# Kernel optimization log

Hardware: AMD Instinct MI355X
Metric: run time of the kernel (lower is better)

The kernel has to match this reference:

```python
import jax, jax.numpy as jnp
import numpy as np

EMBED = 1024
HEADS = 16
HEAD_DIM = EMBED // HEADS


def setup_inputs() -> dict:
    key = jax.random.key(0)
    ks = jax.random.split(key, 8)
    N, S, E = 4, 2048, EMBED
    s = 1.0 / np.sqrt(E)
    return {
        "values": jax.random.normal(ks[0], (N, S, E), jnp.float32),
        "keys": jax.random.normal(ks[1], (N, S, E), jnp.float32),
        "queries": jax.random.normal(ks[2], (N, S, E), jnp.float32),
        # nn.Linear weights stored as (out_features, in_features)
        "Wv": jax.random.normal(ks[3], (E, E), jnp.float32) * s,
        "Wk": jax.random.normal(ks[4], (E, E), jnp.float32) * s,
        "Wq": jax.random.normal(ks[5], (E, E), jnp.float32) * s,
        "Wo": jax.random.normal(ks[6], (E, E), jnp.float32) * s,
        "bo": jax.random.normal(ks[7], (E,), jnp.float32) * s,
    }


def reference(values, keys, queries, Wv, Wk, Wq, Wo, bo):
    N = queries.shape[0]
    H, D, E = HEADS, HEAD_DIM, EMBED
    # projections (torch Linear: x @ W.T), reshape to [N, S, H, D]
    v = (values @ Wv.T).reshape(N, -1, H, D)
    k = (keys @ Wk.T).reshape(N, -1, H, D)
    q = (queries @ Wq.T).reshape(N, -1, H, D)
    energy = jnp.einsum("nqhd,nkhd->nhqk", q, k)
    # NOTE: original scales by sqrt(embed_size), not sqrt(head_dim)
    attn = jax.nn.softmax(energy / jnp.sqrt(jnp.float32(E)), axis=3)
    out = jnp.einsum("nhql,nlhd->nqhd", attn, v).reshape(N, -1, H * D)
    return out @ Wo.T + bo
```

## Files before the change

### kernel.cpp

```cpp
#include <hip/hip_runtime.h>

typedef __bf16  bf16x8 __attribute__((ext_vector_type(8)));
typedef float   f32x4  __attribute__((ext_vector_type(4)));
typedef unsigned short u16x8 __attribute__((ext_vector_type(8)));

__device__ __forceinline__ unsigned short f2bf(float f) {
    union { float f; unsigned int u; } v; v.f = f;
    unsigned int u = v.u;
    unsigned int r = (u + 0x7fffu + ((u >> 16) & 1u)) >> 16;
    return (unsigned short)r;
}

__device__ __forceinline__ unsigned int pkbf(float lo, float hi) {
    union { float f; unsigned int u; } a, b; a.f = lo; b.f = hi;
    return __builtin_amdgcn_perm(b.u + 0x8000u, a.u + 0x8000u, 0x07060302u);
}

__device__ __forceinline__ void gld_lds16(const unsigned short* g, unsigned short* l) {
    auto gp = (const __attribute__((address_space(1))) unsigned int*)(const void*)g;
    auto lp = (__attribute__((address_space(3))) unsigned int*)(unsigned int)(unsigned long long)(void*)l;
    __builtin_amdgcn_global_load_lds(gp, lp, 16, 0, 0);
}

__global__ void cast4_kernel(const float* __restrict__ a, const float* __restrict__ b,
                             const float* __restrict__ c, const float* __restrict__ d,
                             unsigned short* __restrict__ dst) {
    int sel = blockIdx.x >> 10;
    int off4 = (blockIdx.x & 1023) * 256 + threadIdx.x;
    const float* src = sel == 0 ? a : sel == 1 ? b : sel == 2 ? c : d;
    float4 f = ((const float4*)src)[off4];
    uint2 pk; pk.x = pkbf(f.x, f.y); pk.y = pkbf(f.z, f.w);
    ((uint2*)(dst + (size_t)sel * 1048576))[off4] = pk;
}

__global__ void cast_kernel(const float* __restrict__ src, unsigned short* __restrict__ dst, int n4) {
    int stride = gridDim.x * 256;
    for (int i = blockIdx.x * 256 + threadIdx.x; i < n4; i += stride) {
        float4 f = ((const float4*)src)[i];
        uint2 pk; pk.x = pkbf(f.x, f.y); pk.y = pkbf(f.z, f.w);
        ((uint2*)dst)[i] = pk;
    }
}

template <int MODE>
__global__ __launch_bounds__(256, 3)
void gemm_bt(const unsigned short* __restrict__ A, const unsigned short* __restrict__ Bt,
             void* __restrict__ dst, const float* __restrict__ bias, float a_scale)
{
    constexpr int K = 1024;
    __shared__ unsigned short As[2][4096];
    __shared__ unsigned short Bs[2][4096];

    const int t    = threadIdx.x;
    const int lane = t & 63;
    const int w    = t >> 6;
    const int q    = lane >> 4;
    const int ln   = lane & 15;
    const int wr   = w >> 1, wc = w & 1;
    const int m0   = blockIdx.x * 128;
    const int n0   = blockIdx.y * 128;
    const int srow = lane >> 2;
    const int scol = (lane & 3) * 8;

    f32x4 acc[4][4];
    const f32x4 zz = {0.f, 0.f, 0.f, 0.f};
#pragma unroll
    for (int i = 0; i < 4; ++i)
#pragma unroll
        for (int j = 0; j < 4; ++j) acc[i][j] = zz;

    auto stage = [&](int k0, int p) {
#pragma unroll
        for (int c = 0; c < 2; ++c) {
            int u = w * 2 + c;
            gld_lds16(A  + (size_t)(m0 + u * 16 + srow) * K + k0 + scol, &As[p][u * 512]);
            gld_lds16(Bt + (size_t)(n0 + u * 16 + srow) * K + k0 + scol, &Bs[p][u * 512]);
        }
    };

    stage(0, 0);
    for (int j = 0; j < 32; ++j) {
        __syncthreads();
        if (j < 31) stage((j + 1) * 32, (j + 1) & 1);
        const int p = j & 1;
        bf16x8 af[4], bfr[4];
#pragma unroll
        for (int i = 0; i < 4; ++i)
            af[i] = *(const bf16x8*)&As[p][(wr * 64 + i * 16 + ln) * 32 + q * 8];
#pragma unroll
        for (int jj = 0; jj < 4; ++jj)
            bfr[jj] = *(const bf16x8*)&Bs[p][(wc * 64 + jj * 16 + ln) * 32 + q * 8];
#pragma unroll
        for (int i = 0; i < 4; ++i)
#pragma unroll
            for (int jj = 0; jj < 4; ++jj)
                acc[i][jj] = __builtin_amdgcn_mfma_f32_16x16x32_bf16(af[i], bfr[jj], acc[i][jj], 0, 0, 0);
    }

#pragma unroll
    for (int i = 0; i < 4; ++i) {
#pragma unroll
        for (int j = 0; j < 4; ++j) {
            f32x4 c = acc[i][j];
            int mb = m0 + wr * 64 + i * 16 + q * 4;
            int nn = n0 + wc * 64 + j * 16 + ln;
            if constexpr (MODE == 1) {
                int b = mb >> 11, s = mb & 2047, h = nn >> 6, d = nn & 63;
                uint2 pk;
                pk.x = pkbf(c[0], c[1]);
                pk.y = pkbf(c[2], c[3]);
                size_t idx = (((size_t)(b * 16 + h) * 64) + d) * 2048 + s;
                *(uint2*)&((unsigned short*)dst)[idx] = pk;
            } else {
#pragma unroll
                for (int r = 0; r < 4; ++r) {
                    int m = mb + r;
                    float val = c[r] * a_scale;
                    if constexpr (MODE == 2) {
                        ((float*)dst)[(size_t)m * 1024 + nn] = val + bias[nn];
                    } else {
                        int b = m >> 11, s = m & 2047, h = nn >> 6, d = nn & 63;
                        size_t idx = (((size_t)(b * 16 + h) * 2048) + s) * 64 + d;
                        ((unsigned short*)dst)[idx] = f2bf(val);
                    }
                }
            }
        }
    }
}

__global__ __launch_bounds__(256, 3)
void attn_kernel(const unsigned short* __restrict__ Q, const unsigned short* __restrict__ Kg,
                 const unsigned short* __restrict__ Vt, unsigned short* __restrict__ Og)
{
    __shared__ unsigned short Ks[2][4096];
    __shared__ unsigned short Vs[2][4096];
    __shared__ unsigned short Ps[128 * 72];

    const int t    = threadIdx.x;
    const int lane = t & 63;
    const int w    = t >> 6;
    const int q    = lane >> 4;
    const int ln   = lane & 15;
    const int head = blockIdx.x;
    const int qt   = blockIdx.y;

    const unsigned short* Qh  = Q  + (size_t)head * 2048 * 64;
    const unsigned short* Kh  = Kg + (size_t)head * 2048 * 64;
    const unsigned short* Vth = Vt + (size_t)head * 64 * 2048;

    const int srow = lane >> 2;
    const int scol = (lane & 3) * 8;

    bf16x8 qf[2][2];
    const int rowb = qt * 128 + w * 32;
#pragma unroll
    for (int ti = 0; ti < 2; ++ti)
#pragma unroll
        for (int kc = 0; kc < 2; ++kc)
            qf[ti][kc] = *(const bf16x8*)&Qh[(size_t)(rowb + ti * 16 + ln) * 64 + kc * 32 + q * 8];

    const f32x4 zz = {0.f, 0.f, 0.f, 0.f};
    f32x4 oa[2][4];
#pragma unroll
    for (int ti = 0; ti < 2; ++ti)
#pragma unroll
        for (int dt = 0; dt < 4; ++dt) oa[ti][dt] = zz;
    float l_s[2] = {0.f, 0.f};

    auto stage = [&](int j, int p) {
#pragma unroll
        for (int c = 0; c < 2; ++c) {
            int u = w * 2 + c;
            int kc = u >> 2, rg = u & 3;
            gld_lds16(Kh + (size_t)(j * 64 + rg * 16 + srow) * 64 + kc * 32 + scol,
                      &Ks[p][kc * 2048 + rg * 512]);
            gld_lds16(Vth + (size_t)(rg * 16 + srow) * 2048 + j * 64 + kc * 32 + scol,
                      &Vs[p][kc * 2048 + rg * 512]);
        }
    };

    stage(0, 0);
    for (int j = 0; j < 32; ++j) {
        __syncthreads();
        if (j < 31) stage(j + 1, (j + 1) & 1);
        const int p = j & 1;

        f32x4 sa[4][2];
#pragma unroll
        for (int kt = 0; kt < 4; ++kt)
#pragma unroll
            for (int ti = 0; ti < 2; ++ti) sa[kt][ti] = zz;
#pragma unroll
        for (int kc = 0; kc < 2; ++kc) {
            bf16x8 ka[4];
#pragma unroll
            for (int kt = 0; kt < 4; ++kt)
                ka[kt] = *(const bf16x8*)&Ks[p][kc * 2048 + (kt * 16 + ln) * 32 + q * 8];
#pragma unroll
            for (int kt = 0; kt < 4; ++kt)
#pragma unroll
                for (int ti = 0; ti < 2; ++ti)
                    sa[kt][ti] = __builtin_amdgcn_mfma_f32_16x16x32_bf16(ka[kt], qf[ti][kc], sa[kt][ti], 0, 0, 0);
        }

#pragma unroll
        for (int ti = 0; ti < 2; ++ti) {
            float rs = 0.f;
            const int prow = w * 32 + ti * 16 + ln;
#pragma unroll
            for (int kt = 0; kt < 4; ++kt) {
                float p0 = exp2f(sa[kt][ti][0]);
                float p1 = exp2f(sa[kt][ti][1]);
                float p2 = exp2f(sa[kt][ti][2]);
                float p3 = exp2f(sa[kt][ti][3]);
                rs += (p0 + p1) + (p2 + p3);
                uint2 pk;
                pk.x = pkbf(p0, p1);
                pk.y = pkbf(p2, p3);
                *(uint2*)&Ps[prow * 72 + kt * 16 + q * 4] = pk;
            }
            rs += __shfl_xor(rs, 16);
            rs += __shfl_xor(rs, 32);
            l_s[ti] += rs;
        }

#pragma unroll
        for (int kc = 0; kc < 2; ++kc) {
            bf16x8 va[4], pb[2];
#pragma unroll
            for (int dt = 0; dt < 4; ++dt)
                va[dt] = *(const bf16x8*)&Vs[p][kc * 2048 + (dt * 16 + ln) * 32 + q * 8];
#pragma unroll
            for (int ti = 0; ti < 2; ++ti)
                pb[ti] = *(const bf16x8*)&Ps[(w * 32 + ti * 16 + ln) * 72 + kc * 32 + q * 8];
#pragma unroll
            for (int ti = 0; ti < 2; ++ti)
#pragma unroll
                for (int dt = 0; dt < 4; ++dt)
                    oa[ti][dt] = __builtin_amdgcn_mfma_f32_16x16x32_bf16(va[dt], pb[ti], oa[ti][dt], 0, 0, 0);
        }
    }

    const int n = head >> 4;
    const int hbase = (head & 15) * 64;
#pragma unroll
    for (int ti = 0; ti < 2; ++ti) {
        float inv = 1.f / l_s[ti];
        int sr = qt * 128 + w * 32 + ti * 16 + ln;
        size_t base = ((size_t)n * 2048 + sr) * 1024 + hbase;
#pragma unroll
        for (int dt = 0; dt < 4; ++dt) {
            uint2 pk;
            pk.x = pkbf(oa[ti][dt][0] * inv, oa[ti][dt][1] * inv);
            pk.y = pkbf(oa[ti][dt][2] * inv, oa[ti][dt][3] * inv);
            *(uint2*)&Og[base + dt * 16 + q * 4] = pk;
        }
    }
}

extern "C" void kernel_launch(void* const* d_in, const int* in_sizes, int n_in,
                              void* d_out, int out_size, void* d_ws, size_t ws_size,
                              hipStream_t stream)
{
    (void)in_sizes; (void)n_in; (void)out_size; (void)ws_size;
    const float* values  = (const float*)d_in[0];
    const float* keys    = (const float*)d_in[1];
    const float* queries = (const float*)d_in[2];
    const float* Wv = (const float*)d_in[3];
    const float* Wk = (const float*)d_in[4];
    const float* Wq = (const float*)d_in[5];
    const float* Wo = (const float*)d_in[6];
    const float* bo = (const float*)d_in[7];
    float* out = (float*)d_out;

    unsigned short* ws   = (unsigned short*)d_ws;
    unsigned short* Wv_b = ws;
    unsigned short* Wk_b = ws + 1048576;
    unsigned short* Wq_b = ws + 2097152;
    unsigned short* Wo_b = ws + 3145728;
    unsigned short* Act  = ws + 4194304;
    unsigned short* Ob   = Act;
    unsigned short* Qb   = ws + 12582912;
    unsigned short* Kb   = Qb + 8388608;
    unsigned short* Vtb  = Kb + 8388608;

    cast4_kernel<<<4096, 256, 0, stream>>>(Wv, Wk, Wq, Wo, ws);

    dim3 g(64, 8), b(256);
    const float qscale = 1.4426950408889634f / 32.f;

    cast_kernel<<<4096, 256, 0, stream>>>(values, Act, 2097152);
    gemm_bt<1><<<g, b, 0, stream>>>(Act, Wv_b, Vtb, nullptr, 1.f);
    cast_kernel<<<4096, 256, 0, stream>>>(keys, Act, 2097152);
    gemm_bt<0><<<g, b, 0, stream>>>(Act, Wk_b, Kb, nullptr, 1.f);
    cast_kernel<<<4096, 256, 0, stream>>>(queries, Act, 2097152);
    gemm_bt<0><<<g, b, 0, stream>>>(Act, Wq_b, Qb, nullptr, qscale);

    attn_kernel<<<dim3(64, 16), b, 0, stream>>>(Qb, Kb, Vtb, Ob);
    gemm_bt<2><<<g, b, 0, stream>>>(Ob, Wo_b, out, bo, 1.f);
}
```

Before: 370.2 us.

## Keep softmax probabilities in registers and swizzle K/V shared-memory layout

Removes the Ps shared-memory staging buffer by feeding exp'd scores straight from the QK MFMA accumulators into 16x16x16 bf16 MFMAs for the PV product. It also XOR-swizzles the K/V tiles in LDS to avoid bank conflicts and raises the occupancy hint from 3 to 5 blocks per CU. This cuts LDS traffic and a write/read round trip per tile. The trade is twice as many smaller-K MFMA instructions for PV, plus round-to-nearest conversion via convertvector.

```diff
diff --git a/kernel.cpp b/kernel.cpp
--- a/kernel.cpp
+++ b/kernel.cpp
@@ -1,6 +1,8 @@
 #include <hip/hip_runtime.h>
 
 typedef __bf16  bf16x8 __attribute__((ext_vector_type(8)));
+typedef __bf16  bf16x4 __attribute__((ext_vector_type(4)));
+typedef short   s16x4  __attribute__((ext_vector_type(4)));
 typedef float   f32x4  __attribute__((ext_vector_type(4)));
 typedef unsigned short u16x8 __attribute__((ext_vector_type(8)));
 
@@ -20,6 +22,18 @@
     auto gp = (const __attribute__((address_space(1))) unsigned int*)(const void*)g;
     auto lp = (__attribute__((address_space(3))) unsigned int*)(unsigned int)(unsigned long long)(void*)l;
     __builtin_amdgcn_global_load_lds(gp, lp, 16, 0, 0);
+}
+
+__device__ __forceinline__ f32x4 mfma16(bf16x4 a, bf16x4 b, f32x4 c) {
+#if __has_builtin(__builtin_amdgcn_mfma_f32_16x16x16_bf16)
+    return __builtin_amdgcn_mfma_f32_16x16x16_bf16(a, b, c, 0, 0, 0);
+#elif __has_builtin(__builtin_amdgcn_mfma_f32_16x16x16bf16_1k)
+    union U { bf16x4 h; s16x4 s; } ua, ub; ua.h = a; ub.h = b;
+    return __builtin_amdgcn_mfma_f32_16x16x16bf16_1k(ua.s, ub.s, c, 0, 0, 0);
+#else
+    asm("v_mfma_f32_16x16x16_bf16 %0, %1, %2, %0" : "+v"(c) : "v"(a), "v"(b));
+    return c;
+#endif
 }
 
 __global__ void cast4_kernel(const float* __restrict__ a, const float* __restrict__ b,
@@ -129,19 +143,19 @@
     }
 }
 
-__global__ __launch_bounds__(256, 3)
+__global__ __launch_bounds__(256, 5)
 void attn_kernel(const unsigned short* __restrict__ Q, const unsigned short* __restrict__ Kg,
                  const unsigned short* __restrict__ Vt, unsigned short* __restrict__ Og)
 {
-    __shared__ unsigned short Ks[2][4096];
-    __shared__ unsigned short Vs[2][4096];
-    __shared__ unsigned short Ps[128 * 72];
+    __shared__ __align__(16) unsigned short Ks[2][4096];
+    __shared__ __align__(16) unsigned short Vs[2][4096];
 
     const int t    = threadIdx.x;
     const int lane = t & 63;
     const int w    = t >> 6;
     const int q    = lane >> 4;
     const int ln   = lane & 15;
+    const int xs   = (ln >> 1) & 3;
     const int head = blockIdx.x;
     const int qt   = blockIdx.y;
 
@@ -150,7 +164,7 @@
     const unsigned short* Vth = Vt + (size_t)head * 64 * 2048;
 
     const int srow = lane >> 2;
-    const int scol = (lane & 3) * 8;
+    const int ssw  = ((lane & 3) ^ ((lane >> 3) & 3)) * 8;
 
     bf16x8 qf[2][2];
     const int rowb = qt * 128 + w * 32;
@@ -173,9 +187,9 @@
         for (int c = 0; c < 2; ++c) {
             int u = w * 2 + c;
             int kc = u >> 2, rg = u & 3;
-            gld_lds16(Kh + (size_t)(j * 64 + rg * 16 + srow) * 64 + kc * 32 + scol,
+            gld_lds16(Kh + (size_t)(j * 64 + rg * 16 + srow) * 64 + kc * 32 + ssw,
                       &Ks[p][kc * 2048 + rg * 512]);
-            gld_lds16(Vth + (size_t)(rg * 16 + srow) * 2048 + j * 64 + kc * 32 + scol,
+            gld_lds16(Vth + (size_t)(rg * 16 + srow) * 2048 + j * 64 + kc * 32 + ssw,
                       &Vs[p][kc * 2048 + rg * 512]);
         }
     };
@@ -186,59 +200,46 @@
         if (j < 31) stage(j + 1, (j + 1) & 1);
         const int p = j & 1;
 
-        f32x4 sa[4][2];
-#pragma unroll
-        for (int kt = 0; kt < 4; ++kt)
-#pragma unroll
-            for (int ti = 0; ti < 2; ++ti) sa[kt][ti] = zz;
-#pragma unroll
-        for (int kc = 0; kc < 2; ++kc) {
-            bf16x8 ka[4];
-#pragma unroll
-            for (int kt = 0; kt < 4; ++kt)
-                ka[kt] = *(const bf16x8*)&Ks[p][kc * 2048 + (kt * 16 + ln) * 32 + q * 8];
-#pragma unroll
-            for (int kt = 0; kt < 4; ++kt)
-#pragma unroll
-                for (int ti = 0; ti < 2; ++ti)
-                    sa[kt][ti] = __builtin_amdgcn_mfma_f32_16x16x32_bf16(ka[kt], qf[ti][kc], sa[kt][ti], 0, 0, 0);
-        }
-
-#pragma unroll
-        for (int ti = 0; ti < 2; ++ti) {
-            float rs = 0.f;
-            const int prow = w * 32 + ti * 16 + ln;
-#pragma unroll
-            for (int kt = 0; kt < 4; ++kt) {
-                float p0 = exp2f(sa[kt][ti][0]);
-                float p1 = exp2f(sa[kt][ti][1]);
-                float p2 = exp2f(sa[kt][ti][2]);
-                float p3 = exp2f(sa[kt][ti][3]);
-                rs += (p0 + p1) + (p2 + p3);
-                uint2 pk;
-                pk.x = pkbf(p0, p1);
-                pk.y = pkbf(p2, p3);
-                *(uint2*)&Ps[prow * 72 + kt * 16 + q * 4] = pk;
-            }
-            rs += __shfl_xor(rs, 16);
-            rs += __shfl_xor(rs, 32);
-            l_s[ti] += rs;
-        }
-
-#pragma unroll
-        for (int kc = 0; kc < 2; ++kc) {
-            bf16x8 va[4], pb[2];
+        bf16x4 pb[4][2];
+        float rs0 = 0.f, rs1 = 0.f;
+#pragma unroll
+        for (int kt = 0; kt < 4; ++kt) {
+            f32x4 s0 = zz, s1 = zz;
+#pragma unroll
+            for (int kc = 0; kc < 2; ++kc) {
+                bf16x8 ka = *(const bf16x8*)&Ks[p][kc * 2048 + (kt * 16 + ln) * 32 + ((q ^ xs) * 8)];
+                s0 = __builtin_amdgcn_mfma_f32_16x16x32_bf16(ka, qf[0][kc], s0, 0, 0, 0);
+                s1 = __builtin_amdgcn_mfma_f32_16x16x32_bf16(ka, qf[1][kc], s1, 0, 0, 0);
+            }
+            {
+                float a0 = exp2f(s0[0]), a1 = exp2f(s0[1]), a2 = exp2f(s0[2]), a3 = exp2f(s0[3]);
+                rs0 += (a0 + a1) + (a2 + a3);
+                f32x4 pe = {a0, a1, a2, a3};
+                pb[kt][0] = __builtin_convertvector(pe, bf16x4);
+            }
+            {
+                float b0 = exp2f(s1[0]), b1 = exp2f(s1[1]), b2 = exp2f(s1[2]), b3 = exp2f(s1[3]);
+                rs1 += (b0 + b1) + (b2 + b3);
+                f32x4 pe = {b0, b1, b2, b3};
+                pb[kt][1] = __builtin_convertvector(pe, bf16x4);
+            }
+        }
+        rs0 += __shfl_xor(rs0, 16); rs0 += __shfl_xor(rs0, 32); l_s[0] += rs0;
+        rs1 += __shfl_xor(rs1, 16); rs1 += __shfl_xor(rs1, 32); l_s[1] += rs1;
+
+#pragma unroll
+        for (int kt = 0; kt < 4; ++kt) {
+            const int kc = kt >> 1;
+            const int so = ((((kt & 1) * 2 + (q >> 1)) ^ xs) * 8) + (q & 1) * 4;
+            bf16x4 va[4];
 #pragma unroll
             for (int dt = 0; dt < 4; ++dt)
-                va[dt] = *(const bf16x8*)&Vs[p][kc * 2048 + (dt * 16 + ln) * 32 + q * 8];
-#pragma unroll
-            for (int ti = 0; ti < 2; ++ti)
-                pb[ti] = *(const bf16x8*)&Ps[(w * 32 + ti * 16 + ln) * 72 + kc * 32 + q * 8];
-#pragma unroll
-            for (int ti = 0; ti < 2; ++ti)
-#pragma unroll
-                for (int dt = 0; dt < 4; ++dt)
-                    oa[ti][dt] = __builtin_amdgcn_mfma_f32_16x16x32_bf16(va[dt], pb[ti], oa[ti][dt], 0, 0, 0);
+                va[dt] = *(const bf16x4*)&Vs[p][kc * 2048 + (dt * 16 + ln) * 32 + so];
+#pragma unroll
+            for (int dt = 0; dt < 4; ++dt) {
+                oa[0][dt] = mfma16(va[dt], pb[kt][0], oa[0][dt]);
+                oa[1][dt] = mfma16(va[dt], pb[kt][1], oa[1][dt]);
+            }
         }
     }
 
```

After: 460.7 us. 24.5% more time.
